# Optimization experiments

Hardware: AMD Instinct MI355X
Metric: run time of the kernel (lower is better)

Reference implementation:

```python
import jax, jax.numpy as jnp
import numpy as np

B, S, E = 2, 2048, 2048
H, D = 16, 128  # num_attention_heads, head_dim = hidden_size // num_heads


def rotate_half(x):
    x1 = x[..., : x.shape[-1] // 2]
    x2 = x[..., x.shape[-1] // 2 :]
    return jnp.concatenate((-x2, x1), axis=-1)


def setup_inputs() -> dict:
    key = jax.random.key(0)
    ks = jax.random.split(key, 7)
    return {
        "hidden_states": jax.random.normal(ks[0], (B, S, E), dtype=jnp.float32),
        "cos": jax.random.uniform(ks[1], (1, 1, S, D), dtype=jnp.float32),
        "sin": jax.random.uniform(ks[2], (1, 1, S, D), dtype=jnp.float32),
        "wq": jax.random.normal(ks[3], (E, H * D), dtype=jnp.float32) / np.sqrt(E),
        "wk": jax.random.normal(ks[4], (E, H * D), dtype=jnp.float32) / np.sqrt(E),
        "wv": jax.random.normal(ks[5], (E, H * D), dtype=jnp.float32) / np.sqrt(E),
        "wo": jax.random.normal(ks[6], (H * D, E), dtype=jnp.float32) / np.sqrt(H * D),
    }


def reference(hidden_states, cos, sin, wq, wk, wv, wo):
    # QKV projections (no bias, per attention_bias=False)
    q = (hidden_states @ wq).reshape(B, S, H, D).transpose(0, 2, 1, 3)  # bhsd
    k = (hidden_states @ wk).reshape(B, S, H, D).transpose(0, 2, 1, 3)
    v = (hidden_states @ wv).reshape(B, S, H, D).transpose(0, 2, 1, 3)
    # RoPE (applied after the head transpose, as in the original)
    q = q * cos + rotate_half(q) * sin
    k = k * cos + rotate_half(k) * sin
    # NOTE: original forward never applies self.scaling and uses no causal mask.
    scores = jnp.einsum("bhqd,bhkd->bhqk", q, k)
    attn = jax.nn.softmax(scores.astype(jnp.float32), axis=-1)
    out = jnp.einsum("bhqk,bhkd->bhqd", attn, v)
    out = out.transpose(0, 2, 1, 3).reshape(B, S, H * D)
    return out @ wo
```

## Files before the change

### kernel.cpp

```cpp
#include <hip/hip_runtime.h>
#include <stdint.h>

typedef _Float16 f16;
typedef _Float16 half8 __attribute__((ext_vector_type(8)));
typedef _Float16 half4 __attribute__((ext_vector_type(4)));
typedef __fp16 fp16x2 __attribute__((ext_vector_type(2)));
typedef float f32x4 __attribute__((ext_vector_type(4)));
typedef float f32x16 __attribute__((ext_vector_type(16)));
typedef uint32_t u32x4 __attribute__((ext_vector_type(4)));

static constexpr int Bsz = 2, S = 2048, E = 2048, H = 16, D = 128;
static constexpr int M = Bsz * S;
static constexpr int N_QKV = 3 * H * D;
static constexpr int HD = H * D;

__device__ __forceinline__ void gload_lds16(const void* gp, void* lp) {
  __builtin_amdgcn_global_load_lds(
      (const __attribute__((address_space(1))) uint32_t*)(uintptr_t)gp,
      (__attribute__((address_space(3))) uint32_t*)(uint32_t)(uintptr_t)lp,
      16, 0, 0);
}

__device__ __forceinline__ uint32_t pkrtz(float a, float b) {
  fp16x2 r = __builtin_amdgcn_cvt_pkrtz(a, b);
  return __builtin_bit_cast(uint32_t, r);
}

__global__ void cast_f32_f16(const float* __restrict__ in, f16* __restrict__ out) {
  size_t i = (size_t)(blockIdx.x * 256 + threadIdx.x) * 8;
  float4 a = *(const float4*)&in[i];
  float4 b = *(const float4*)&in[i + 4];
  half8 h;
  h[0] = (f16)a.x; h[1] = (f16)a.y; h[2] = (f16)a.z; h[3] = (f16)a.w;
  h[4] = (f16)b.x; h[5] = (f16)b.y; h[6] = (f16)b.z; h[7] = (f16)b.w;
  *(half8*)&out[i] = h;
}

__global__ void transpose_cast(const float* __restrict__ wq, const float* __restrict__ wk,
                               const float* __restrict__ wv, const float* __restrict__ wo,
                               f16* __restrict__ wt, f16* __restrict__ wot) {
  __shared__ float tile[32][33];
  int z = blockIdx.z;
  const float* src = (z == 0) ? wq : (z == 1) ? wk : (z == 2) ? wv : wo;
  f16* dst = (z == 3) ? wot : wt + (size_t)z * E * HD;
  int bx = blockIdx.x * 32, by = blockIdx.y * 32;
  int tx = threadIdx.x, ty = threadIdx.y;
#pragma unroll
  for (int r = 0; r < 4; ++r)
    tile[ty + r * 8][tx] = src[(size_t)(by + ty + r * 8) * 2048 + bx + tx];
  __syncthreads();
#pragma unroll
  for (int r = 0; r < 4; ++r)
    dst[(size_t)(bx + ty + r * 8) * 2048 + by + tx] = (f16)tile[tx][ty + r * 8];
}

template <typename OutT>
__global__ __launch_bounds__(256, 4) void gemm_bt(const f16* __restrict__ A,
                                                  const f16* __restrict__ Bt,
                                                  OutT* __restrict__ C,
                                                  int Mm, int Nn, int Kk) {
  __shared__ f16 As[128 * 32];
  __shared__ f16 Bs[128 * 32];
  const int t = threadIdx.x, l = t & 63;
  const int wm = (t >> 7) & 1, wn = (t >> 6) & 1;
  const int bm = blockIdx.x, bn = blockIdx.y;
  const int lr = l & 15, g = l >> 4;
  const int srow = t >> 2;
  const int schunk = t & 3;
  const int scol = ((schunk ^ (srow & 3)) * 8);
  const size_t abase = (size_t)(bm * 128 + srow) * Kk;
  const size_t bbase = (size_t)(bn * 128 + srow) * Kk;
  f32x4 acc[4][4] = {};
  for (int k0 = 0; k0 < Kk; k0 += 32) {
    __syncthreads();
    gload_lds16(&A[abase + k0 + scol], &As[t * 8]);
    gload_lds16(&A[abase + (size_t)64 * Kk + k0 + scol], &As[2048 + t * 8]);
    gload_lds16(&Bt[bbase + k0 + scol], &Bs[t * 8]);
    gload_lds16(&Bt[bbase + (size_t)64 * Kk + k0 + scol], &Bs[2048 + t * 8]);
    __syncthreads();
    half8 af[4], bf[4];
#pragma unroll
    for (int i = 0; i < 4; ++i) {
      int ra = wm * 64 + i * 16 + lr;
      int rb = wn * 64 + i * 16 + lr;
      af[i] = *(const half8*)&As[ra * 32 + ((g ^ (ra & 3)) * 8)];
      bf[i] = *(const half8*)&Bs[rb * 32 + ((g ^ (rb & 3)) * 8)];
    }
#pragma unroll
    for (int i = 0; i < 4; ++i)
#pragma unroll
      for (int j = 0; j < 4; ++j)
        acc[i][j] = __builtin_amdgcn_mfma_f32_16x16x32_f16(af[i], bf[j], acc[i][j], 0, 0, 0);
  }
#pragma unroll
  for (int i = 0; i < 4; ++i)
#pragma unroll
    for (int j = 0; j < 4; ++j) {
      int row = bm * 128 + wm * 64 + i * 16 + g * 4;
      int col = bn * 128 + wn * 64 + j * 16 + lr;
#pragma unroll
      for (int r = 0; r < 4; ++r)
        C[(size_t)(row + r) * Nn + col] = (OutT)acc[i][j][r];
    }
}

__global__ void rope_split(const f16* __restrict__ qkv, const float* __restrict__ cosb,
                           const float* __restrict__ sinb, f16* __restrict__ Q,
                           f16* __restrict__ Ko) {
  int idx = blockIdx.x * 256 + threadIdx.x;
  int d4 = idx & 15;
  int h = (idx >> 4) & 15;
  int s = (idx >> 8) & 2047;
  int b = idx >> 19;
  int d = d4 * 4;
  size_t mrow = (size_t)(b * S + s) * N_QKV;
  const f16* q = &qkv[mrow + h * D];
  const f16* k = &qkv[mrow + HD + h * D];
  size_t ob = ((size_t)(b * H + h) * S + s) * D;
  float4 c1 = *(const float4*)&cosb[s * D + d];
  float4 c2 = *(const float4*)&cosb[s * D + 64 + d];
  float4 s1 = *(const float4*)&sinb[s * D + d];
  float4 s2 = *(const float4*)&sinb[s * D + 64 + d];
  float c1a[4] = {c1.x, c1.y, c1.z, c1.w}, c2a[4] = {c2.x, c2.y, c2.z, c2.w};
  float s1a[4] = {s1.x, s1.y, s1.z, s1.w}, s2a[4] = {s2.x, s2.y, s2.z, s2.w};
  half4 qlo = *(const half4*)&q[d], qhi = *(const half4*)&q[d + 64];
  half4 klo = *(const half4*)&k[d], khi = *(const half4*)&k[d + 64];
  half4 oql, oqh, okl, okh;
#pragma unroll
  for (int j = 0; j < 4; ++j) {
    float ql = (float)qlo[j], qh = (float)qhi[j];
    float kl = (float)klo[j], kh = (float)khi[j];
    oql[j] = (f16)(ql * c1a[j] - qh * s1a[j]);
    oqh[j] = (f16)(qh * c2a[j] + ql * s2a[j]);
    okl[j] = (f16)(kl * c1a[j] - kh * s1a[j]);
    okh[j] = (f16)(kh * c2a[j] + kl * s2a[j]);
  }
  *(half4*)&Q[ob + d] = oql;  *(half4*)&Q[ob + d + 64] = oqh;
  *(half4*)&Ko[ob + d] = okl; *(half4*)&Ko[ob + d + 64] = okh;
}

__global__ void transpose_v(const f16* __restrict__ qkv, f16* __restrict__ VtG) {
  __shared__ f16 tl[64][136];
  int bid = blockIdx.x;
  int bh = bid >> 5, st = bid & 31;
  int b = bh >> 4, h = bh & 15;
  int t = threadIdx.x;
  int s0 = st * 64;
#pragma unroll
  for (int rnd = 0; rnd < 4; ++rnd) {
    int row = rnd * 16 + (t >> 4);
    int ch = t & 15;
    half8 v = *(const half8*)&qkv[(size_t)(b * S + s0 + row) * N_QKV + 2 * HD + h * D + ch * 8];
    *(half8*)&tl[row][ch * 8] = v;
  }
  __syncthreads();
#pragma unroll
  for (int rnd = 0; rnd < 4; ++rnd) {
    int d = rnd * 32 + (t >> 3);
    int ch = t & 7;
    half8 v;
#pragma unroll
    for (int j = 0; j < 8; ++j) v[j] = tl[ch * 8 + j][d];
    *(half8*)&VtG[((size_t)bh * D + d) * S + s0 + ch * 8] = v;
  }
}

__device__ __forceinline__ void stage_kv(const f16* __restrict__ Kg, const f16* __restrict__ Vg,
                                         f16* KsB, f16* VsB, int t, int kv) {
#pragma unroll
  for (int rnd = 0; rnd < 4; ++rnd) {
    int row = rnd * 16 + (t >> 4);
    int c = t & 15;
    gload_lds16(&Kg[(size_t)(kv + row) * D + ((c ^ (row & 7)) * 8)], &KsB[rnd * 2048 + t * 8]);
  }
#pragma unroll
  for (int rnd = 0; rnd < 4; ++rnd) {
    int row = rnd * 32 + (t >> 3);
    int c = t & 7;
    gload_lds16(&Vg[(size_t)row * S + kv + ((c ^ (row & 7)) * 8)], &VsB[rnd * 2048 + t * 8]);
  }
}

__global__ __launch_bounds__(256, 2) void flash_attn2(const f16* __restrict__ Q,
                                                      const f16* __restrict__ K,
                                                      const f16* __restrict__ Vt,
                                                      f16* __restrict__ O) {
  __shared__ f16 lds[2][16384];
  const int t = threadIdx.x, l = t & 63, w = t >> 6;
  const int c = l & 31, hi = l >> 5;
  int bid = blockIdx.x;
  bid = (bid & 7) * 64 + (bid >> 3);
  const int bh = bid >> 4, qt = bid & 15;
  const size_t baseQ = (size_t)bh * S * D;
  const f16* Kg = K + baseQ;
  const f16* Vg = Vt + (size_t)bh * D * S;
  const int q0 = qt * 128 + w * 32;
  half8 qf[8];
#pragma unroll
  for (int dc = 0; dc < 8; ++dc)
    qf[dc] = *(const half8*)&Q[baseQ + (size_t)(q0 + c) * D + dc * 16 + hi * 8];
  f32x16 o[4] = {};
  float m = -3.0e38f, ssum = 0.f;

  stage_kv(Kg, Vg, &lds[0][0], &lds[0][8192], t, 0);
  __syncthreads();

  for (int it = 0; it < S / 64; ++it) {
    const int cur = it & 1;
    const f16* KsB = &lds[cur][0];
    const f16* VsB = &lds[cur][8192];
    if (it + 1 < S / 64) stage_kv(Kg, Vg, &lds[cur ^ 1][0], &lds[cur ^ 1][8192], t, (it + 1) * 64);

    f32x16 s0 = {}, s1 = {};
    __builtin_amdgcn_s_setprio(1);
#pragma unroll
    for (int dc = 0; dc < 8; ++dc) {
      const int r0 = c, r1 = 32 + c;
      half8 kf0 = *(const half8*)&KsB[r0 * 128 + (((2 * dc + hi) ^ (r0 & 7)) * 8)];
      half8 kf1 = *(const half8*)&KsB[r1 * 128 + (((2 * dc + hi) ^ (r1 & 7)) * 8)];
      s0 = __builtin_amdgcn_mfma_f32_32x32x16_f16(kf0, qf[dc], s0, 0, 0, 0);
      s1 = __builtin_amdgcn_mfma_f32_32x32x16_f16(kf1, qf[dc], s1, 0, 0, 0);
    }
    __builtin_amdgcn_s_setprio(0);

    float tm = s0[0];
#pragma unroll
    for (int r = 1; r < 16; ++r) tm = fmaxf(tm, s0[r]);
#pragma unroll
    for (int r = 0; r < 16; ++r) tm = fmaxf(tm, s1[r]);
    tm = fmaxf(tm, __shfl_xor(tm, 32));
    float mn = fmaxf(m, tm);
    float corr = __expf(m - mn);
    m = mn;
    float ts = 0.f;
#pragma unroll
    for (int r = 0; r < 16; ++r) { s0[r] = __expf(s0[r] - mn); ts += s0[r]; }
#pragma unroll
    for (int r = 0; r < 16; ++r) { s1[r] = __expf(s1[r] - mn); ts += s1[r]; }
    ts += __shfl_xor(ts, 32);
    ssum = ssum * corr + ts;
#pragma unroll
    for (int dt = 0; dt < 4; ++dt)
#pragma unroll
      for (int r = 0; r < 16; ++r) o[dt][r] *= corr;

    half8 pf[4];
#pragma unroll
    for (int ks = 0; ks < 4; ++ks) {
      const int B0 = 2 * (ks & 1), B1 = B0 + 1;
      uint32_t X0, X1, Y0, Y1;
      if (ks < 2) {
        X0 = pkrtz(s0[4 * B0 + 0], s0[4 * B0 + 1]);
        X1 = pkrtz(s0[4 * B0 + 2], s0[4 * B0 + 3]);
        Y0 = pkrtz(s0[4 * B1 + 0], s0[4 * B1 + 1]);
        Y1 = pkrtz(s0[4 * B1 + 2], s0[4 * B1 + 3]);
      } else {
        X0 = pkrtz(s1[4 * B0 + 0], s1[4 * B0 + 1]);
        X1 = pkrtz(s1[4 * B0 + 2], s1[4 * B0 + 3]);
        Y0 = pkrtz(s1[4 * B1 + 0], s1[4 * B1 + 1]);
        Y1 = pkrtz(s1[4 * B1 + 2], s1[4 * B1 + 3]);
      }
      asm volatile("v_permlane32_swap_b32 %0, %1" : "+v"(X0), "+v"(Y0));
      asm volatile("v_permlane32_swap_b32 %0, %1" : "+v"(X1), "+v"(Y1));
      u32x4 pw; pw[0] = X0; pw[1] = X1; pw[2] = Y0; pw[3] = Y1;
      pf[ks] = __builtin_bit_cast(half8, pw);
    }

    __builtin_amdgcn_s_setprio(1);
#pragma unroll
    for (int dt = 0; dt < 4; ++dt) {
      const int row = dt * 32 + c;
#pragma unroll
      for (int ks = 0; ks < 4; ++ks) {
        half8 vf = *(const half8*)&VsB[row * 64 + (((2 * ks + hi) ^ (row & 7)) * 8)];
        o[dt] = __builtin_amdgcn_mfma_f32_32x32x16_f16(vf, pf[ks], o[dt], 0, 0, 0);
      }
    }
    __builtin_amdgcn_s_setprio(0);
    __syncthreads();
  }

  const float inv = 1.f / ssum;
  const int b = bh >> 4, h = bh & 15;
  const size_t orow = ((size_t)(b * S + q0 + c)) * HD + h * D;
#pragma unroll
  for (int dt = 0; dt < 4; ++dt)
#pragma unroll
    for (int b2 = 0; b2 < 4; ++b2) {
      half4 h4;
#pragma unroll
      for (int a = 0; a < 4; ++a) h4[a] = (f16)(o[dt][4 * b2 + a] * inv);
      *(half4*)&O[orow + dt * 32 + 8 * b2 + 4 * hi] = h4;
    }
}

extern "C" void kernel_launch(void* const* d_in, const int* in_sizes, int n_in,
                              void* d_out, int out_size, void* d_ws, size_t ws_size,
                              hipStream_t stream) {
  (void)in_sizes; (void)n_in; (void)out_size; (void)ws_size;
  const float* hs = (const float*)d_in[0];
  const float* cosb = (const float*)d_in[1];
  const float* sinb = (const float*)d_in[2];
  const float* wq = (const float*)d_in[3];
  const float* wk = (const float*)d_in[4];
  const float* wv = (const float*)d_in[5];
  const float* wo = (const float*)d_in[6];
  float* out = (float*)d_out;
  char* ws = (char*)d_ws;
  f16* hs16 = (f16*)(ws);
  f16* attn = (f16*)(ws);
  f16* wt   = (f16*)(ws + (16u << 20));
  f16* wot  = (f16*)(ws + (40u << 20));
  f16* qkv  = (f16*)(ws + (48u << 20));
  f16* Qb   = (f16*)(ws + (96u << 20));
  f16* Kb   = (f16*)(ws + (112u << 20));
  f16* VtG  = (f16*)(ws + (128u << 20));

  cast_f32_f16<<<dim3(4096), dim3(256), 0, stream>>>(hs, hs16);
  transpose_cast<<<dim3(64, 64, 4), dim3(32, 8), 0, stream>>>(wq, wk, wv, wo, wt, wot);
  gemm_bt<f16><<<dim3(32, 48), dim3(256), 0, stream>>>(hs16, wt, qkv, M, N_QKV, E);
  rope_split<<<dim3(4096), dim3(256), 0, stream>>>(qkv, cosb, sinb, Qb, Kb);
  transpose_v<<<dim3(1024), dim3(256), 0, stream>>>(qkv, VtG);
  flash_attn2<<<dim3(512), dim3(256), 0, stream>>>(Qb, Kb, VtG, attn);
  gemm_bt<float><<<dim3(32, 16), dim3(256), 0, stream>>>(attn, wot, out, M, E, HD);
}
```

Measured before the change: 308.8 us.

## Replace GEMM with 8-wave double-buffered 128x256 tile kernel with XCD-aware block remap

Replaces the simple single-buffered 128x128 GEMM with a 512-thread kernel computing 128x256 tiles. It double-buffers K=64 steps in LDS, issuing the next tile's global-to-LDS loads while MFMAs run, using explicit vmcnt waits and barriers. Block IDs are remapped across the 8 XCDs, and the LDS swizzle and setprio hints are adjusted. The aim is to hide global load latency and raise data reuse per tile, at the cost of more LDS per block (96KB) and fewer workgroups (768 and 256), which may hurt occupancy and tail balance.

New measurement: 310.0 us. Within noise of the previous version (+0.4%).

```diff
diff --git a/kernel.cpp b/kernel.cpp
--- a/kernel.cpp
+++ b/kernel.cpp
@@ -55,53 +55,106 @@
 }
 
 template <typename OutT>
-__global__ __launch_bounds__(256, 4) void gemm_bt(const f16* __restrict__ A,
-                                                  const f16* __restrict__ Bt,
-                                                  OutT* __restrict__ C,
-                                                  int Mm, int Nn, int Kk) {
-  __shared__ f16 As[128 * 32];
-  __shared__ f16 Bs[128 * 32];
-  const int t = threadIdx.x, l = t & 63;
-  const int wm = (t >> 7) & 1, wn = (t >> 6) & 1;
-  const int bm = blockIdx.x, bn = blockIdx.y;
+__global__ __launch_bounds__(512, 2) void gemm8p(const f16* __restrict__ A,
+                                                 const f16* __restrict__ Bt,
+                                                 OutT* __restrict__ C,
+                                                 int Nn, int Kk, int nbn) {
+  __shared__ f16 lds[49152];
+  const int t = threadIdx.x, l = t & 63, wvid = t >> 6;
+  const int wm = wvid >> 2, wn = wvid & 3;
   const int lr = l & 15, g = l >> 4;
+  const int nwg = gridDim.x;
+  const int bid = blockIdx.x;
+  const int wg = (bid & 7) * (nwg >> 3) + (bid >> 3);
+  const int bm = wg / nbn, bn = wg % nbn;
   const int srow = t >> 2;
-  const int schunk = t & 3;
-  const int scol = ((schunk ^ (srow & 3)) * 8);
-  const size_t abase = (size_t)(bm * 128 + srow) * Kk;
-  const size_t bbase = (size_t)(bn * 128 + srow) * Kk;
+  const int sq = t & 3;
+  const int ssw = ((srow >> 2) ^ srow) & 3;
+  const int scol = (sq ^ ssw) * 8;
+  const int rsw = (((lr >> 2) ^ lr) & 3);
+  const f16* Ab = A + (size_t)(bm * 128 + srow) * Kk + scol;
+  const f16* Bb0 = Bt + (size_t)(bn * 256 + srow) * Kk + scol;
+  const f16* Bb1 = Bt + (size_t)(bn * 256 + 128 + srow) * Kk + scol;
+  const int NT = Kk >> 6;
+
+#define SEC_A(b_, kh_) ((b_) * 24576 + (kh_) * 4096)
+#define SEC_B(b_, kh_) ((b_) * 24576 + 8192 + (kh_) * 8192)
+#define STAGE_SEC(kt_, kh_, b_)                                         \
+  do {                                                                  \
+    int kc_ = (kt_) * 64 + (kh_) * 32;                                  \
+    gload_lds16(Ab + kc_, &lds[SEC_A(b_, kh_) + t * 8]);                \
+    gload_lds16(Bb0 + kc_, &lds[SEC_B(b_, kh_) + t * 8]);               \
+    gload_lds16(Bb1 + kc_, &lds[SEC_B(b_, kh_) + 4096 + t * 8]);        \
+  } while (0)
+#define LDAB(kh_)                                                            \
+  _Pragma("unroll") for (int i = 0; i < 4; ++i) {                            \
+    int ra = wm * 64 + i * 16 + lr;                                          \
+    a[i] = *(const half8*)&lds[SEC_A(cb, kh_) + ra * 32 + (g ^ rsw) * 8];    \
+  }                                                                          \
+  _Pragma("unroll") for (int j = 0; j < 4; ++j) {                            \
+    int rb = wn * 64 + j * 16 + lr;                                          \
+    b[j] = *(const half8*)&lds[SEC_B(cb, kh_) + rb * 32 + (g ^ rsw) * 8];    \
+  }
+#define MFMA16()                                                             \
+  __builtin_amdgcn_s_setprio(1);                                             \
+  _Pragma("unroll") for (int i = 0; i < 4; ++i)                              \
+  _Pragma("unroll") for (int j = 0; j < 4; ++j)                              \
+      acc[i][j] = __builtin_amdgcn_mfma_f32_16x16x32_f16(a[i], b[j], acc[i][j], 0, 0, 0); \
+  __builtin_amdgcn_s_setprio(0);
+#define BAR() __builtin_amdgcn_s_barrier()
+#define VMCNT(n_) asm volatile("s_waitcnt vmcnt(" #n_ ")" ::: "memory")
+#define PREMFMA()                                     \
+  asm volatile("s_waitcnt lgkmcnt(0)" ::: "memory");  \
+  __builtin_amdgcn_sched_barrier(0)
+
   f32x4 acc[4][4] = {};
-  for (int k0 = 0; k0 < Kk; k0 += 32) {
-    __syncthreads();
-    gload_lds16(&A[abase + k0 + scol], &As[t * 8]);
-    gload_lds16(&A[abase + (size_t)64 * Kk + k0 + scol], &As[2048 + t * 8]);
-    gload_lds16(&Bt[bbase + k0 + scol], &Bs[t * 8]);
-    gload_lds16(&Bt[bbase + (size_t)64 * Kk + k0 + scol], &Bs[2048 + t * 8]);
-    __syncthreads();
-    half8 af[4], bf[4];
-#pragma unroll
-    for (int i = 0; i < 4; ++i) {
-      int ra = wm * 64 + i * 16 + lr;
-      int rb = wn * 64 + i * 16 + lr;
-      af[i] = *(const half8*)&As[ra * 32 + ((g ^ (ra & 3)) * 8)];
-      bf[i] = *(const half8*)&Bs[rb * 32 + ((g ^ (rb & 3)) * 8)];
-    }
-#pragma unroll
-    for (int i = 0; i < 4; ++i)
-#pragma unroll
-      for (int j = 0; j < 4; ++j)
-        acc[i][j] = __builtin_amdgcn_mfma_f32_16x16x32_f16(af[i], bf[j], acc[i][j], 0, 0, 0);
-  }
+  STAGE_SEC(0, 0, 0);
+  STAGE_SEC(0, 1, 0);
+  VMCNT(3);
+  BAR();
+
+  for (int kt = 0; kt < NT; ++kt) {
+    const int cb = kt & 1;
+    half8 a[4], b[4];
+    LDAB(0);
+    if (kt + 1 < NT) {
+      STAGE_SEC(kt + 1, 0, cb ^ 1);
+      VMCNT(3);
+    } else {
+      VMCNT(0);
+    }
+    BAR();
+    PREMFMA();
+    MFMA16();
+    BAR();
+    LDAB(1);
+    if (kt + 1 < NT) {
+      STAGE_SEC(kt + 1, 1, cb ^ 1);
+      VMCNT(3);
+    }
+    BAR();
+    PREMFMA();
+    MFMA16();
+    BAR();
+  }
+
+  const int crow = bm * 128 + wm * 64 + g * 4;
+  const int ccol = bn * 256 + wn * 64 + lr;
 #pragma unroll
   for (int i = 0; i < 4; ++i)
 #pragma unroll
-    for (int j = 0; j < 4; ++j) {
-      int row = bm * 128 + wm * 64 + i * 16 + g * 4;
-      int col = bn * 128 + wn * 64 + j * 16 + lr;
+    for (int j = 0; j < 4; ++j)
 #pragma unroll
       for (int r = 0; r < 4; ++r)
-        C[(size_t)(row + r) * Nn + col] = (OutT)acc[i][j][r];
-    }
+        C[(size_t)(crow + i * 16 + r) * Nn + ccol + j * 16] = (OutT)acc[i][j][r];
+#undef SEC_A
+#undef SEC_B
+#undef STAGE_SEC
+#undef LDAB
+#undef MFMA16
+#undef BAR
+#undef VMCNT
+#undef PREMFMA
 }
 
 __global__ void rope_split(const f16* __restrict__ qkv, const float* __restrict__ cosb,
@@ -318,9 +371,9 @@
 
   cast_f32_f16<<<dim3(4096), dim3(256), 0, stream>>>(hs, hs16);
   transpose_cast<<<dim3(64, 64, 4), dim3(32, 8), 0, stream>>>(wq, wk, wv, wo, wt, wot);
-  gemm_bt<f16><<<dim3(32, 48), dim3(256), 0, stream>>>(hs16, wt, qkv, M, N_QKV, E);
+  gemm8p<f16><<<dim3(32 * 24), dim3(512), 0, stream>>>(hs16, wt, qkv, N_QKV, E, 24);
   rope_split<<<dim3(4096), dim3(256), 0, stream>>>(qkv, cosb, sinb, Qb, Kb);
   transpose_v<<<dim3(1024), dim3(256), 0, stream>>>(qkv, VtG);
   flash_attn2<<<dim3(512), dim3(256), 0, stream>>>(Qb, Kb, VtG, attn);
-  gemm_bt<float><<<dim3(32, 16), dim3(256), 0, stream>>>(attn, wot, out, M, E, HD);
-}
+  gemm8p<float><<<dim3(32 * 8), dim3(512), 0, stream>>>(attn, wot, out, E, HD, 8);
+}
```

## Fuse RoPE, head split and V transpose into QKV GEMM epilogue

Applied to the files above, without the earlier changes.

Replaces the separate QKV GEMM, rope_split and transpose_v kernels with one GEMM whose epilogue writes Q and K with RoPE applied in head-major layout, and writes V transposed directly. The intent is to drop the intermediate qkv buffer's write and re-read plus two kernel launches. In exchange the epilogue needs extra LDS staging (32KB shared), which may lower occupancy, and the transposed V stores are narrower and strided.

New measurement: 312.2 us. Within noise of the previous version (+1.1%).

```diff
diff --git a/kernel.cpp b/kernel.cpp
--- a/kernel.cpp
+++ b/kernel.cpp
@@ -52,6 +52,114 @@
 #pragma unroll
   for (int r = 0; r < 4; ++r)
     dst[(size_t)(bx + ty + r * 8) * 2048 + by + tx] = (f16)tile[tx][ty + r * 8];
+}
+
+__global__ __launch_bounds__(256, 4) void qkv_fused(const f16* __restrict__ A,
+                                                    const f16* __restrict__ Bt,
+                                                    const float* __restrict__ cosb,
+                                                    const float* __restrict__ sinb,
+                                                    f16* __restrict__ Qb,
+                                                    f16* __restrict__ Kb,
+                                                    f16* __restrict__ VtG) {
+  __shared__ f16 lds[16384];
+  f16* As = lds;
+  f16* Bs = lds + 4096;
+  const int Kk = E;
+  const int t = threadIdx.x, l = t & 63;
+  const int wm = (t >> 7) & 1, wn = (t >> 6) & 1;
+  const int bm = blockIdx.x, bn = blockIdx.y;
+  const int lr = l & 15, g = l >> 4;
+  const int srow = t >> 2;
+  const int schunk = t & 3;
+  const int scol = ((schunk ^ (srow & 3)) * 8);
+  const size_t abase = (size_t)(bm * 128 + srow) * Kk;
+  const size_t bbase = (size_t)(bn * 128 + srow) * Kk;
+  f32x4 acc[4][4] = {};
+  for (int k0 = 0; k0 < Kk; k0 += 32) {
+    __syncthreads();
+    gload_lds16(&A[abase + k0 + scol], &As[t * 8]);
+    gload_lds16(&A[abase + (size_t)64 * Kk + k0 + scol], &As[2048 + t * 8]);
+    gload_lds16(&Bt[bbase + k0 + scol], &Bs[t * 8]);
+    gload_lds16(&Bt[bbase + (size_t)64 * Kk + k0 + scol], &Bs[2048 + t * 8]);
+    __syncthreads();
+    half8 af[4], bf[4];
+#pragma unroll
+    for (int i = 0; i < 4; ++i) {
+      int ra = wm * 64 + i * 16 + lr;
+      int rb = wn * 64 + i * 16 + lr;
+      af[i] = *(const half8*)&As[ra * 32 + ((g ^ (ra & 3)) * 8)];
+      bf[i] = *(const half8*)&Bs[rb * 32 + ((g ^ (rb & 3)) * 8)];
+    }
+#pragma unroll
+    for (int i = 0; i < 4; ++i)
+#pragma unroll
+      for (int j = 0; j < 4; ++j)
+        acc[i][j] = __builtin_amdgcn_mfma_f32_16x16x32_f16(af[i], bf[j], acc[i][j], 0, 0, 0);
+  }
+
+  const int bt = bn >> 4;
+  const int h = bn & 15;
+  const int b = bm >> 4;
+  const int bh = b * 16 + h;
+  const int sblk = (bm & 15) * 128;
+
+  if (bt == 2) {
+#pragma unroll
+    for (int j = 0; j < 4; ++j) {
+      int d = wn * 64 + j * 16 + lr;
+      size_t rowb = ((size_t)bh * D + d) * S;
+#pragma unroll
+      for (int i = 0; i < 4; ++i) {
+        int s0 = sblk + wm * 64 + i * 16 + g * 4;
+        half4 h4;
+#pragma unroll
+        for (int r = 0; r < 4; ++r) h4[r] = (f16)acc[i][j][r];
+        *(half4*)&VtG[rowb + s0] = h4;
+      }
+    }
+  } else {
+    __syncthreads();
+#pragma unroll
+    for (int i = 0; i < 4; ++i)
+#pragma unroll
+      for (int j = 0; j < 4; ++j) {
+        int row = wm * 64 + i * 16 + g * 4;
+        int col = wn * 64 + j * 16 + lr;
+#pragma unroll
+        for (int r = 0; r < 4; ++r) lds[(row + r) * 128 + col] = (f16)acc[i][j][r];
+      }
+    __syncthreads();
+    f16* Dst = (bt == 0) ? Qb : Kb;
+    const int r2 = t >> 1;
+    const int sg = sblk + r2;
+    const size_t obase = ((size_t)bh * S + sg) * D;
+    const size_t cbase = (size_t)sg * D;
+#pragma unroll
+    for (int k = 0; k < 4; ++k) {
+      const int dd0 = (t & 1) * 32 + k * 8;
+#pragma unroll
+      for (int half = 0; half < 2; ++half) {
+        const int dd = dd0 + half * 4;
+        float4 cl = *(const float4*)&cosb[cbase + dd];
+        float4 ch = *(const float4*)&cosb[cbase + dd + 64];
+        float4 sl = *(const float4*)&sinb[cbase + dd];
+        float4 sh = *(const float4*)&sinb[cbase + dd + 64];
+        half4 lo = *(half4*)&lds[r2 * 128 + dd];
+        half4 hv = *(half4*)&lds[r2 * 128 + dd + 64];
+        half4 olo, ohi;
+        olo[0] = (f16)((float)lo[0] * cl.x - (float)hv[0] * sl.x);
+        olo[1] = (f16)((float)lo[1] * cl.y - (float)hv[1] * sl.y);
+        olo[2] = (f16)((float)lo[2] * cl.z - (float)hv[2] * sl.z);
+        olo[3] = (f16)((float)lo[3] * cl.w - (float)hv[3] * sl.w);
+        ohi[0] = (f16)((float)hv[0] * ch.x + (float)lo[0] * sh.x);
+        ohi[1] = (f16)((float)hv[1] * ch.y + (float)lo[1] * sh.y);
+        ohi[2] = (f16)((float)hv[2] * ch.z + (float)lo[2] * sh.z);
+        ohi[3] = (f16)((float)hv[3] * ch.w + (float)lo[3] * sh.w);
+        *(half4*)&Dst[obase + dd] = olo;
+        *(half4*)&Dst[obase + dd + 64] = ohi;
+      }
+    }
+  }
 }
 
 template <typename OutT>
@@ -104,67 +212,6 @@
     }
 }
 
-__global__ void rope_split(const f16* __restrict__ qkv, const float* __restrict__ cosb,
-                           const float* __restrict__ sinb, f16* __restrict__ Q,
-                           f16* __restrict__ Ko) {
-  int idx = blockIdx.x * 256 + threadIdx.x;
-  int d4 = idx & 15;
-  int h = (idx >> 4) & 15;
-  int s = (idx >> 8) & 2047;
-  int b = idx >> 19;
-  int d = d4 * 4;
-  size_t mrow = (size_t)(b * S + s) * N_QKV;
-  const f16* q = &qkv[mrow + h * D];
-  const f16* k = &qkv[mrow + HD + h * D];
-  size_t ob = ((size_t)(b * H + h) * S + s) * D;
-  float4 c1 = *(const float4*)&cosb[s * D + d];
-  float4 c2 = *(const float4*)&cosb[s * D + 64 + d];
-  float4 s1 = *(const float4*)&sinb[s * D + d];
-  float4 s2 = *(const float4*)&sinb[s * D + 64 + d];
-  float c1a[4] = {c1.x, c1.y, c1.z, c1.w}, c2a[4] = {c2.x, c2.y, c2.z, c2.w};
-  float s1a[4] = {s1.x, s1.y, s1.z, s1.w}, s2a[4] = {s2.x, s2.y, s2.z, s2.w};
-  half4 qlo = *(const half4*)&q[d], qhi = *(const half4*)&q[d + 64];
-  half4 klo = *(const half4*)&k[d], khi = *(const half4*)&k[d + 64];
-  half4 oql, oqh, okl, okh;
-#pragma unroll
-  for (int j = 0; j < 4; ++j) {
-    float ql = (float)qlo[j], qh = (float)qhi[j];
-    float kl = (float)klo[j], kh = (float)khi[j];
-    oql[j] = (f16)(ql * c1a[j] - qh * s1a[j]);
-    oqh[j] = (f16)(qh * c2a[j] + ql * s2a[j]);
-    okl[j] = (f16)(kl * c1a[j] - kh * s1a[j]);
-    okh[j] = (f16)(kh * c2a[j] + kl * s2a[j]);
-  }
-  *(half4*)&Q[ob + d] = oql;  *(half4*)&Q[ob + d + 64] = oqh;
-  *(half4*)&Ko[ob + d] = okl; *(half4*)&Ko[ob + d + 64] = okh;
-}
-
-__global__ void transpose_v(const f16* __restrict__ qkv, f16* __restrict__ VtG) {
-  __shared__ f16 tl[64][136];
-  int bid = blockIdx.x;
-  int bh = bid >> 5, st = bid & 31;
-  int b = bh >> 4, h = bh & 15;
-  int t = threadIdx.x;
-  int s0 = st * 64;
-#pragma unroll
-  for (int rnd = 0; rnd < 4; ++rnd) {
-    int row = rnd * 16 + (t >> 4);
-    int ch = t & 15;
-    half8 v = *(const half8*)&qkv[(size_t)(b * S + s0 + row) * N_QKV + 2 * HD + h * D + ch * 8];
-    *(half8*)&tl[row][ch * 8] = v;
-  }
-  __syncthreads();
-#pragma unroll
-  for (int rnd = 0; rnd < 4; ++rnd) {
-    int d = rnd * 32 + (t >> 3);
-    int ch = t & 7;
-    half8 v;
-#pragma unroll
-    for (int j = 0; j < 8; ++j) v[j] = tl[ch * 8 + j][d];
-    *(half8*)&VtG[((size_t)bh * D + d) * S + s0 + ch * 8] = v;
-  }
-}
-
 __device__ __forceinline__ void stage_kv(const f16* __restrict__ Kg, const f16* __restrict__ Vg,
                                          f16* KsB, f16* VsB, int t, int kv) {
 #pragma unroll
@@ -311,16 +358,13 @@
   f16* attn = (f16*)(ws);
   f16* wt   = (f16*)(ws + (16u << 20));
   f16* wot  = (f16*)(ws + (40u << 20));
-  f16* qkv  = (f16*)(ws + (48u << 20));
-  f16* Qb   = (f16*)(ws + (96u << 20));
-  f16* Kb   = (f16*)(ws + (112u << 20));
-  f16* VtG  = (f16*)(ws + (128u << 20));
+  f16* Qb   = (f16*)(ws + (48u << 20));
+  f16* Kb   = (f16*)(ws + (64u << 20));
+  f16* VtG  = (f16*)(ws + (80u << 20));
 
   cast_f32_f16<<<dim3(4096), dim3(256), 0, stream>>>(hs, hs16);
   transpose_cast<<<dim3(64, 64, 4), dim3(32, 8), 0, stream>>>(wq, wk, wv, wo, wt, wot);
-  gemm_bt<f16><<<dim3(32, 48), dim3(256), 0, stream>>>(hs16, wt, qkv, M, N_QKV, E);
-  rope_split<<<dim3(4096), dim3(256), 0, stream>>>(qkv, cosb, sinb, Qb, Kb);
-  transpose_v<<<dim3(1024), dim3(256), 0, stream>>>(qkv, VtG);
+  qkv_fused<<<dim3(32, 48), dim3(256), 0, stream>>>(hs16, wt, cosb, sinb, Qb, Kb, VtG);
   flash_attn2<<<dim3(512), dim3(256), 0, stream>>>(Qb, Kb, VtG, attn);
   gemm_bt<float><<<dim3(32, 16), dim3(256), 0, stream>>>(attn, wot, out, M, E, HD);
 }
```
